# Kernel tuning notes

Hardware: AMD Instinct MI355X
Metric: run time of the kernel (lower is better)

## Reference

```python
import jax, jax.numpy as jnp
import numpy as np

B, D, CIN, H, W = 2, 6, 3, 96, 96
DIM, NUM_HEADS, DEPTH = 144, 6, 2
WS = (2, 8, 8)   # window size (d, h, w)
SS = (1, 4, 4)   # shift size for odd blocks
HID = int(DIM * 2.0)
TBL = (2 * WS[0] - 1) * (2 * WS[1] - 1) * (2 * WS[2] - 1)  # 675
EPS = 1e-5


def _rpi(ws):
    # pairwise relative position index, same math as WindowAttention.get_position_index
    coords = np.stack(np.meshgrid(np.arange(ws[0]), np.arange(ws[1]), np.arange(ws[2]), indexing='ij'))
    cf = coords.reshape(3, -1).astype(np.int64)
    rc = (cf[:, :, None] - cf[:, None, :]).transpose(1, 2, 0)
    rc[..., 0] += ws[0] - 1
    rc[..., 1] += ws[1] - 1
    rc[..., 2] += ws[2] - 1
    rc[..., 0] *= (2 * ws[1] - 1) * (2 * ws[2] - 1)
    rc[..., 1] *= 2 * ws[2] - 1
    return rc.sum(-1)  # (N, N)


def _win_part_np(x, ws):
    b, d, h, w, c = x.shape
    x = x.reshape(b, d // ws[0], ws[0], h // ws[1], ws[1], w // ws[2], ws[2], c)
    return x.transpose(0, 1, 3, 5, 2, 4, 6, 7).reshape(-1, ws[0] * ws[1] * ws[2], c)


def _attn_mask(Dp, Hp, Wp, ws, ss):
    # static shift-window attention mask, same as compute_mask
    img = np.zeros((1, Dp, Hp, Wp, 1), np.float32)
    cnt = 0
    for d in (slice(-ws[0]), slice(-ws[0], -ss[0]), slice(-ss[0], None)):
        for h in (slice(-ws[1]), slice(-ws[1], -ss[1]), slice(-ss[1], None)):
            for w in (slice(-ws[2]), slice(-ws[2], -ss[2]), slice(-ss[2], None)):
                img[:, d, h, w, :] = cnt
                cnt += 1
    mw = _win_part_np(img, ws)[..., 0]  # (nW, N)
    am = mw[:, None, :] - mw[:, :, None]
    return np.where(am != 0, np.float32(-100.0), np.float32(0.0))


RPI = jnp.asarray(_rpi(WS))            # (N, N) int
MASK = jnp.asarray(_attn_mask(D, H, W, WS, SS))  # (nW, N, N)


def _ln(x, g, b):
    mu = jnp.mean(x, -1, keepdims=True)
    var = jnp.mean(jnp.square(x - mu), -1, keepdims=True)
    return (x - mu) * jax.lax.rsqrt(var + EPS) * g + b


def _win_part(x, ws):
    b, d, h, w, c = x.shape
    x = x.reshape(b, d // ws[0], ws[0], h // ws[1], ws[1], w // ws[2], ws[2], c)
    return x.transpose(0, 1, 3, 5, 2, 4, 6, 7).reshape(-1, ws[0] * ws[1] * ws[2], c)


def _win_rev(xw, ws, b, d, h, w):
    x = xw.reshape(b, d // ws[0], h // ws[1], w // ws[2], ws[0], ws[1], ws[2], -1)
    return x.transpose(0, 1, 4, 2, 5, 3, 6, 7).reshape(b, d, h, w, -1)


def _stl(x, i, shifted, params):
    # one Swin Transformer Layer; x: (B, D, H, W, C)
    n1g, n1b, qkvw, qkvb, rpb, projw, projb, n2g, n2b, fc1w, fc1b, fc2w, fc2b = params
    b, d, h, w, c = x.shape
    hd = c // NUM_HEADS
    scale = hd ** -0.5
    y = _ln(x, n1g[i], n1b[i])
    if shifted:
        y = jnp.roll(y, (-SS[0], -SS[1], -SS[2]), axis=(1, 2, 3))
    xw = _win_part(y, WS)  # (B_, N, C)
    B_, N, _ = xw.shape
    qkv = jnp.einsum('bnc,oc->bno', xw, qkvw[i]) + qkvb[i]
    qkv = qkv.reshape(B_, N, 3, NUM_HEADS, hd).transpose(2, 0, 3, 1, 4)
    q, k, v = qkv[0], qkv[1], qkv[2]
    attn = jnp.einsum('bhnd,bhmd->bhnm', q * scale, k)
    bias = rpb[i][RPI].transpose(2, 0, 1)  # (heads, N, N)
    attn = attn + bias[None]
    if shifted:
        nW = MASK.shape[0]
        attn = attn.reshape(B_ // nW, nW, NUM_HEADS, N, N) + MASK[None, :, None]
        attn = attn.reshape(B_, NUM_HEADS, N, N)
    attn = jax.nn.softmax(attn, axis=-1)
    out = jnp.einsum('bhnm,bhmd->bhnd', attn, v).transpose(0, 2, 1, 3).reshape(B_, N, c)
    out = jnp.einsum('bnc,oc->bno', out, projw[i]) + projb[i]
    y = _win_rev(out, WS, b, d, h, w)
    if shifted:
        y = jnp.roll(y, (SS[0], SS[1], SS[2]), axis=(1, 2, 3))
    x = x + y
    z = _ln(x, n2g[i], n2b[i])
    z = jnp.einsum('bdhwc,oc->bdhwo', z, fc1w[i]) + fc1b[i]
    z = jax.nn.gelu(z, approximate=False)
    z = jnp.einsum('bdhwo,co->bdhwc', z, fc2w[i]) + fc2b[i]
    return x + z


def setup_inputs() -> dict:
    key = jax.random.key(0)
    ks = jax.random.split(key, 8)
    s = 0.02
    return {
        'x': jax.random.normal(ks[0], (B, D, CIN, H, W), jnp.float32),
        'conv_w': jax.random.normal(ks[1], (DIM, CIN, 1, 3, 3), jnp.float32) * s,
        'conv_b': jnp.zeros((DIM,), jnp.float32),
        'ln0_g': jnp.ones((DIM,), jnp.float32),
        'ln0_b': jnp.zeros((DIM,), jnp.float32),
        'n1g': jnp.ones((DEPTH, DIM), jnp.float32),
        'n1b': jnp.zeros((DEPTH, DIM), jnp.float32),
        'qkvw': jax.random.normal(ks[2], (DEPTH, 3 * DIM, DIM), jnp.float32) * s,
        'qkvb': jnp.zeros((DEPTH, 3 * DIM), jnp.float32),
        'rpb': jax.random.normal(ks[3], (DEPTH, TBL, NUM_HEADS), jnp.float32) * s,
        'projw': jax.random.normal(ks[4], (DEPTH, DIM, DIM), jnp.float32) * s,
        'projb': jnp.zeros((DEPTH, DIM), jnp.float32),
        'n2g': jnp.ones((DEPTH, DIM), jnp.float32),
        'n2b': jnp.zeros((DEPTH, DIM), jnp.float32),
        'fc1w': jax.random.normal(ks[5], (DEPTH, HID, DIM), jnp.float32) * s,
        'fc1b': jnp.zeros((DEPTH, HID), jnp.float32),
        'fc2w': jax.random.normal(ks[6], (DEPTH, DIM, HID), jnp.float32) * s,
        'fc2b': jnp.zeros((DEPTH, DIM), jnp.float32),
        'lin_w': jax.random.normal(ks[7], (DIM, DIM), jnp.float32) * s,
        'lin_b': jnp.zeros((DIM,), jnp.float32),
        'ln1_g': jnp.ones((DIM,), jnp.float32),
        'ln1_b': jnp.zeros((DIM,), jnp.float32),
    }


def reference(x, conv_w, conv_b, ln0_g, ln0_b, n1g, n1b, qkvw, qkvb, rpb, projw, projb,
              n2g, n2b, fc1w, fc1b, fc2w, fc2b, lin_w, lin_b, ln1_g, ln1_b):
    # x: (n, d, c, h, w)
    y = x.transpose(0, 2, 1, 3, 4)  # n c d h w
    y = jax.lax.conv_general_dilated(
        y, conv_w, (1, 1, 1), [(0, 0), (1, 1), (1, 1)],
        dimension_numbers=('NCDHW', 'OIDHW', 'NCDHW')) + conv_b[None, :, None, None, None]
    y = y.transpose(0, 2, 3, 4, 1)  # n d h w c
    y = _ln(y, ln0_g, ln0_b)
    y = y.transpose(0, 4, 1, 2, 3)  # n c d h w
    params = (n1g, n1b, qkvw, qkvb, rpb, projw, projb, n2g, n2b, fc1w, fc1b, fc2w, fc2b)
    # RSTB (num_blocks = 1): residual group (STG of DEPTH STLs) + linear + skip
    f = y.transpose(0, 2, 3, 4, 1)  # b d h w c
    for i in range(DEPTH):
        f = _stl(f, i, i % 2 == 1, params)
    f = jnp.einsum('bdhwc,oc->bdhwo', f, lin_w) + lin_b
    y = y + f.transpose(0, 4, 1, 2, 3)
    # trailing LayerNorm and rearrange back to (n, d, c, h, w)
    out = _ln(y.transpose(0, 2, 3, 4, 1), ln1_g, ln1_b)
    return out.transpose(0, 1, 4, 2, 3)
```

## Files before the change

kernel.cpp:

```cpp
#include <hip/hip_runtime.h>
#include <math.h>

#define NTOK 110592
#define NWIN 864
#define TS   15925248

typedef unsigned short u16;
typedef unsigned int   u32;
typedef __attribute__((ext_vector_type(8))) short short8;
typedef __attribute__((ext_vector_type(4))) float float4v;

__device__ __forceinline__ float bf2f(u16 v) { return __uint_as_float(((u32)v) << 16); }
__device__ __forceinline__ u16 f2bf(float f) {
    u32 u = __float_as_uint(f);
    u32 r = u + 0x7fffu + ((u >> 16) & 1u);
    return (u16)(r >> 16);
}
__device__ __forceinline__ void unpack2(u32 u, float& lo, float& hi) {
    lo = __uint_as_float(u << 16);
    hi = __uint_as_float(u & 0xffff0000u);
}
__device__ __forceinline__ u32 pack2(float lo, float hi) {
    return (u32)f2bf(lo) | ((u32)f2bf(hi) << 16);
}
__device__ __forceinline__ float wave_sum(float v) {
    #pragma unroll
    for (int o = 32; o > 0; o >>= 1) v += __shfl_xor(v, o, 64);
    return v;
}

__device__ __forceinline__ void win_to_src(int tw, int shifted, int& sb, int& sd, int& sh, int& sw) {
    int n = tw & 127;
    int win = tw >> 7;
    int ww = win % 12;
    int wh = (win / 12) % 12;
    int rest = win / 144;
    int wd = rest % 3;
    sb = rest / 3;
    int ld = n >> 6, lh = (n >> 3) & 7, lw = n & 7;
    int dr = wd * 2 + ld, hr = wh * 8 + lh, wr = ww * 8 + lw;
    if (shifted) {
        sd = (dr + 1) % 6;
        sh = (hr + 4) % 96;
        sw = (wr + 4) % 96;
    } else {
        sd = dr; sh = hr; sw = wr;
    }
}

__device__ __forceinline__ int tok_region(int t, int wdn, int whn, int wwn) {
    int dr = wdn * 2 + (t >> 6), hr = whn * 8 + ((t >> 3) & 7), wr = wwn * 8 + (t & 7);
    int rd = (dr < 4) ? 0 : ((dr < 5) ? 1 : 2);
    int rh = (hr < 88) ? 0 : ((hr < 92) ? 1 : 2);
    int rw = (wr < 88) ? 0 : ((wr < 92) ? 1 : 2);
    return rd * 9 + rh * 3 + rw;
}

__global__ __launch_bounds__(256) void convert_weights(
    const float* __restrict__ qkvw, const float* __restrict__ projw,
    const float* __restrict__ fc1w, const float* __restrict__ fc2w,
    const float* __restrict__ linw, u16* __restrict__ wbuf,
    const float* __restrict__ rpb, float* __restrict__ bexp)
{
    int i = blockIdx.x * 256 + threadIdx.x;
    if (i < 124416) wbuf[i] = f2bf(qkvw[i]);
    else if (i < 165888) wbuf[i] = f2bf(projw[i - 124416]);
    else if (i < 248832) wbuf[i] = f2bf(fc1w[i - 165888]);
    else if (i < 331776) wbuf[i] = f2bf(fc2w[i - 248832]);
    else if (i < 352512) wbuf[i] = f2bf(linw[i - 331776]);
    else if (i < 549120) {
        int k = i - 352512;
        int n = k & 127, m = (k >> 7) & 127;
        int lh = k >> 14;
        int h = lh % 6, l = lh / 6;
        int rdi = (m >> 6) - (n >> 6) + 1;
        int rhi = ((m >> 3) & 7) - ((n >> 3) & 7) + 7;
        int rwi = (m & 7) - (n & 7) + 7;
        int bi = (rdi * 15 + rhi) * 15 + rwi;
        bexp[k] = rpb[l * 4050 + bi * 6 + h];
    }
}

__global__ __launch_bounds__(256) void conv_ln0_row(
    const float* __restrict__ x, const float* __restrict__ cw, const float* __restrict__ cb,
    const float* __restrict__ g0, const float* __restrict__ b0,
    float* __restrict__ y0)
{
    int bh = blockIdx.x;
    int h = bh % 96, bd = bh / 96;
    int b = bd / 6, d = bd - b * 6;
    __shared__ float ws[192][29];
    __shared__ float xsr[9][100];
    __shared__ float cbias[192], gg[144], bbv[144];
    int tid = threadIdx.x;

    for (int i = tid; i < 9 * 98; i += 256) {
        int row = i / 98, wx = i - row * 98;
        int ci = row / 3, kh = row - 3 * ci;
        int hh = h + kh - 1, wsrc = wx - 1;
        float v = 0.f;
        if (hh >= 0 && hh < 96 && wsrc >= 0 && wsrc < 96)
            v = x[((((size_t)b * 6 + d) * 3 + ci) * 96 + hh) * 96 + wsrc];
        xsr[row][wx] = v;
    }
    for (int i = tid; i < 192 * 27; i += 256) {
        int c = i / 27, j = i - c * 27;
        ws[c][j] = (c < 144) ? cw[c * 27 + j] : 0.f;
    }
    for (int i = tid; i < 192; i += 256) cbias[i] = (i < 144) ? cb[i] : 0.f;
    for (int i = tid; i < 144; i += 256) { gg[i] = g0[i]; bbv[i] = b0[i]; }
    __syncthreads();

    int wv = tid >> 6, lane = tid & 63;
    int p0 = wv * 24;

    float a0[24], a1[24], a2[24];
    #pragma unroll
    for (int k = 0; k < 24; k++) {
        a0[k] = cbias[lane]; a1[k] = cbias[lane + 64]; a2[k] = cbias[lane + 128];
    }

    for (int cikh = 0; cikh < 9; cikh++) {
        const float* xr = &xsr[cikh][p0];
        float xv[26];
        #pragma unroll
        for (int t = 0; t < 26; t++) xv[t] = xr[t];
        #pragma unroll
        for (int kw = 0; kw < 3; kw++) {
            int j = cikh * 3 + kw;
            float w0 = ws[lane][j], w1 = ws[lane + 64][j], w2 = ws[lane + 128][j];
            #pragma unroll
            for (int k = 0; k < 24; k++) {
                float xvv = xv[k + kw];
                a0[k] += w0 * xvv; a1[k] += w1 * xvv; a2[k] += w2 * xvv;
            }
        }
    }

    #pragma unroll
    for (int k = 0; k < 24; k++) {
        int p = p0 + k;
        float v0 = a0[k], v1 = a1[k];
        float v2m = (lane < 16) ? a2[k] : 0.f;
        float s  = wave_sum(v0 + v1 + v2m);
        float s2 = wave_sum(v0 * v0 + v1 * v1 + v2m * v2m);
        float mu = s * (1.f / 144.f);
        float rstd = rsqrtf(fmaxf(s2 * (1.f / 144.f) - mu * mu, 0.f) + 1e-5f);
        size_t o = ((size_t)bh * 96 + p) * 144;
        float r0 = (v0 - mu) * rstd * gg[lane] + bbv[lane];
        float r1 = (v1 - mu) * rstd * gg[lane + 64] + bbv[lane + 64];
        y0[o + lane] = r0;
        y0[o + lane + 64] = r1;
        if (lane < 16) {
            float r2 = (a2[k] - mu) * rstd * gg[lane + 128] + bbv[lane + 128];
            y0[o + lane + 128] = r2;
        }
    }
}

template<int MODE>
__global__ __launch_bounds__(256) void ln_gather(
    const float* __restrict__ in, u16* __restrict__ out,
    const float* __restrict__ g, const float* __restrict__ bt)
{
    int tok = blockIdx.x * 4 + (threadIdx.x >> 6);
    int lane = threadIdx.x & 63;
    int src;
    if (MODE == 0) src = tok;
    else {
        int b, d, h, w;
        win_to_src(tok, MODE == 2, b, d, h, w);
        src = ((b * 6 + d) * 96 + h) * 96 + w;
    }
    const float2* row = (const float2*)(in + (size_t)src * 144);
    float2 a = row[lane];
    float2 b2 = (lane < 8) ? row[64 + lane] : make_float2(0.f, 0.f);
    float s  = wave_sum(a.x + a.y + b2.x + b2.y);
    float s2 = wave_sum(a.x * a.x + a.y * a.y + b2.x * b2.x + b2.y * b2.y);
    float mu = s * (1.f / 144.f);
    float rstd = rsqrtf(fmaxf(s2 * (1.f / 144.f) - mu * mu, 0.f) + 1e-5f);
    const float2* g2 = (const float2*)g;
    const float2* t2 = (const float2*)bt;
    u32* orow = (u32*)(out + (size_t)tok * 144);
    float2 gg = g2[lane], tt = t2[lane];
    orow[lane] = pack2((a.x - mu) * rstd * gg.x + tt.x, (a.y - mu) * rstd * gg.y + tt.y);
    if (lane < 8) {
        float2 gh = g2[64 + lane], th = t2[64 + lane];
        orow[64 + lane] = pack2((b2.x - mu) * rstd * gh.x + th.x, (b2.y - mu) * rstd * gh.y + th.y);
    }
}

template<int AMODE, int EPI, int SHIFTED, int ADDBIAS, int KTILES>
__global__ __launch_bounds__(192) void mgemm(
    const void* __restrict__ Asrc, const u16* __restrict__ Wt, const float* __restrict__ bias,
    u16* __restrict__ outb, float* __restrict__ fres, const float* __restrict__ y0,
    int a_add, int a_ld, int w_ld, int o_ld, int o_add)
{
    __shared__ u16 As[64 * 152];
    int m0 = blockIdx.y * 64, n0 = blockIdx.x * 144;
    int tid = threadIdx.x;
    int wv3 = tid / 64, lane = tid & 63;
    int mrow = lane & 15, quad = lane >> 4;
    const short8 z8 = {0, 0, 0, 0, 0, 0, 0, 0};

    float4v acc[4][3];
    #pragma unroll
    for (int i = 0; i < 4; i++)
        #pragma unroll
        for (int j = 0; j < 3; j++) acc[i][j] = (float4v){0.f, 0.f, 0.f, 0.f};

    #pragma unroll
    for (int kt = 0; kt < KTILES; kt++) {
        if (kt) __syncthreads();
        if (AMODE == 2) {
            const u16* A = (const u16*)Asrc;
            #pragma unroll
            for (int idx = tid; idx < 1152; idx += 192) {
                int r = idx / 18, c4 = idx - r * 18;
                *(short8*)&As[r * 152 + c4 * 8] =
                    *(const short8*)&A[(size_t)(a_add + m0 + r) * a_ld + kt * 144 + c4 * 8];
            }
        } else if (AMODE == 3) {
            const u16* A = (const u16*)Asrc;
            int chtok = a_ld;
            int cc = m0 / chtok;
            int t0 = m0 - cc * chtok;
            const u16* Ac = A + (size_t)cc * chtok * 144;
            #pragma unroll
            for (int idx = tid; idx < 1152; idx += 192) {
                int r = idx / 18, c4 = idx - r * 18;
                int hh = c4 / 3, sub = c4 - hh * 3;
                *(short8*)&As[r * 152 + c4 * 8] =
                    *(const short8*)&Ac[((size_t)hh * chtok + t0 + r) * 24 + sub * 8];
            }
        } else {
            const float* A = (const float*)Asrc;
            #pragma unroll
            for (int idx = tid; idx < 2304; idx += 192) {
                int r = idx / 36, c4 = idx - r * 36;
                const float4* src4 = (const float4*)&A[(size_t)(a_add + m0 + r) * a_ld + kt * 144];
                float4 v = src4[c4];
                *(u32*)&As[r * 152 + c4 * 4]     = pack2(v.x, v.y);
                *(u32*)&As[r * 152 + c4 * 4 + 2] = pack2(v.z, v.w);
            }
        }
        __syncthreads();

        const u16* Wg = Wt + (size_t)(n0 + wv3 * 48 + mrow) * w_ld + kt * 144;

        #pragma unroll
        for (int ks = 0; ks < 4; ks++) {
            int k0 = ks * 32;
            short8 af[4], bf[3];
            #pragma unroll
            for (int i = 0; i < 4; i++)
                af[i] = *(const short8*)&As[(i * 16 + mrow) * 152 + k0 + quad * 8];
            #pragma unroll
            for (int j = 0; j < 3; j++)
                bf[j] = *(const short8*)&Wg[(size_t)j * 16 * w_ld + k0 + quad * 8];
            #pragma unroll
            for (int i = 0; i < 4; i++)
                #pragma unroll
                for (int j = 0; j < 3; j++)
                    acc[i][j] = __builtin_amdgcn_mfma_f32_16x16x32_bf16(af[i], bf[j], acc[i][j], 0, 0, 0);
        }
        {
            bool tl = (quad < 2);
            short8 af[4], bf[3];
            #pragma unroll
            for (int i = 0; i < 4; i++)
                af[i] = tl ? *(const short8*)&As[(i * 16 + mrow) * 152 + 128 + quad * 8] : z8;
            #pragma unroll
            for (int j = 0; j < 3; j++)
                bf[j] = tl ? *(const short8*)&Wg[(size_t)j * 16 * w_ld + 128 + quad * 8] : z8;
            #pragma unroll
            for (int i = 0; i < 4; i++)
                #pragma unroll
                for (int j = 0; j < 3; j++)
                    acc[i][j] = __builtin_amdgcn_mfma_f32_16x16x32_bf16(af[i], bf[j], acc[i][j], 0, 0, 0);
        }
    }

    #pragma unroll
    for (int i = 0; i < 4; i++) {
        #pragma unroll
        for (int reg = 0; reg < 4; reg++) {
            int m = m0 + i * 16 + quad * 4 + reg;
            int orow;
            if (EPI == 2 || EPI == 5) {
                int b, d, h, w;
                win_to_src(m, SHIFTED, b, d, h, w);
                orow = ((b * 6 + d) * 96 + h) * 96 + w;
            } else orow = m + o_add;
            #pragma unroll
            for (int j = 0; j < 3; j++) {
                int n = n0 + wv3 * 48 + j * 16 + mrow;
                float v = acc[i][j][reg];
                if (ADDBIAS) v += bias[n];
                if (EPI == 1) v = 0.5f * v * (1.f + erff(v * 0.70710678118f));
                if (EPI == 2 || EPI == 3) {
                    fres[(size_t)orow * 144 + n] += v;
                } else if (EPI == 5) {
                    fres[(size_t)orow * 144 + n] = y0[(size_t)orow * 144 + n] + v;
                } else if (EPI == 6) {
                    int slot = n / 144;
                    int hn = n - slot * 144;
                    int head = hn / 24, dd = hn - head * 24;
                    if (slot == 0) v *= 0.20412414523193154f;
                    outb[((size_t)head * o_ld + orow) * 72 + slot * 24 + dd] = f2bf(v);
                } else {
                    if (EPI == 4) v += y0[(size_t)orow * o_ld + n];
                    outb[(size_t)orow * o_ld + n] = f2bf(v);
                }
            }
        }
    }
}

template<int SHIFTED>
__global__ __launch_bounds__(256) void attn_mfma(
    const u16* __restrict__ qkv,
    const float* __restrict__ bexp,
    u16* __restrict__ tok_out,
    int win_base, int chtok)
{
    int win = blockIdx.x;
    int head = blockIdx.y;
    __shared__ __align__(16) u16 Pb[4][2048];
    __shared__ __align__(16) u16 Vt[3072];
    __shared__ float invden_s[128];
    __shared__ u32 reg_pack[32];

    int tid = threadIdx.x;
    int wv = tid >> 6, lane = tid & 63;
    int c = lane & 15, quad = lane >> 4;
    int qbase = wv * 32;
    const short8 z8 = {0, 0, 0, 0, 0, 0, 0, 0};
    const float* bh_ = bexp + head * 16384;
    const u16* base = qkv + ((size_t)head * chtok + (size_t)win * 128) * 72;
    int cs = (c & 7) << 3;

    int wdn = 0, whn = 0, wwn = 0;
    if (SHIFTED) {
        int wib = (win_base + win) % 432;
        wwn = wib % 12; whn = (wib / 12) % 12; wdn = wib / 144;
    }

    if (tid < 128) {
        const u32* vsrc = (const u32*)(base + (size_t)tid * 72 + 48);
        #pragma unroll
        for (int i = 0; i < 12; i++) {
            u32 u = vsrc[i];
            int d0 = 2 * i, d1 = 2 * i + 1;
            Vt[((d0 << 7) + tid) ^ ((d0 & 7) << 3)] = (u16)(u & 0xffffu);
            Vt[((d1 << 7) + tid) ^ ((d1 & 7) << 3)] = (u16)(u >> 16);
        }
    }
    if (SHIFTED && tid < 32) {
        int t0 = tid * 4;
        reg_pack[tid] = (u32)tok_region(t0, wdn, whn, wwn)
                      | ((u32)tok_region(t0 + 1, wdn, whn, wwn) << 8)
                      | ((u32)tok_region(t0 + 2, wdn, whn, wwn) << 16)
                      | ((u32)tok_region(t0 + 3, wdn, whn, wwn) << 24);
    }
    __syncthreads();

    short8 aq[2];
    #pragma unroll
    for (int i = 0; i < 2; i++) {
        aq[i] = z8;
        if (quad < 3)
            aq[i] = *(const short8*)(base + (size_t)(qbase + i * 16 + c) * 72 + quad * 8);
    }

    float4v s_acc[2][8];
    #pragma unroll
    for (int i = 0; i < 2; i++)
        #pragma unroll
        for (int j = 0; j < 8; j++) s_acc[i][j] = (float4v){0.f, 0.f, 0.f, 0.f};

    #pragma unroll
    for (int j = 0; j < 8; j++) {
        short8 kf = z8;
        if (quad < 3)
            kf = *(const short8*)(base + (size_t)(j * 16 + c) * 72 + 24 + quad * 8);
        s_acc[0][j] = __builtin_amdgcn_mfma_f32_16x16x32_bf16(kf, aq[0], s_acc[0][j], 0, 0, 0);
        s_acc[1][j] = __builtin_amdgcn_mfma_f32_16x16x32_bf16(kf, aq[1], s_acc[1][j], 0, 0, 0);
    }

    float4v o_acc[2][2];
    #pragma unroll
    for (int i = 0; i < 2; i++)
        #pragma unroll
        for (int jv = 0; jv < 2; jv++) o_acc[i][jv] = (float4v){0.f, 0.f, 0.f, 0.f};

    #pragma unroll
    for (int i = 0; i < 2; i++) {
        int m = qbase + i * 16 + c;
        const float* brow = bh_ + m * 128;
        u32 myreg = SHIFTED ? (u32)tok_region(m, wdn, whn, wwn) : 0u;
        float den = 0.f;
        #pragma unroll
        for (int j = 0; j < 8; j++) {
            float4 bv = *(const float4*)(brow + j * 16 + quad * 4);
            float s0 = s_acc[i][j][0] + bv.x;
            float s1 = s_acc[i][j][1] + bv.y;
            float s2 = s_acc[i][j][2] + bv.z;
            float s3 = s_acc[i][j][3] + bv.w;
            if (SHIFTED) {
                u32 rv = reg_pack[j * 4 + quad];
                s0 += ((rv & 255u) == myreg) ? 0.f : -100.f;
                s1 += (((rv >> 8) & 255u) == myreg) ? 0.f : -100.f;
                s2 += (((rv >> 16) & 255u) == myreg) ? 0.f : -100.f;
                s3 += ((rv >> 24) == myreg) ? 0.f : -100.f;
            }
            float p0 = __expf(s0), p1 = __expf(s1), p2 = __expf(s2), p3 = __expf(s3);
            den += (p0 + p1) + (p2 + p3);
            u32 w0, w1;
            asm("v_cvt_pk_bf16_f32 %0, %1, %2" : "=v"(w0) : "v"(p0), "v"(p1));
            asm("v_cvt_pk_bf16_f32 %0, %1, %2" : "=v"(w1) : "v"(p2), "v"(p3));
            uint2 wpair = make_uint2(w0, w1);
            *(uint2*)&Pb[wv][((c << 7) + j * 16 + quad * 4) ^ cs] = wpair;
        }
        den += __shfl_xor(den, 16, 64);
        den += __shfl_xor(den, 32, 64);
        if (quad == 0) invden_s[m] = 1.f / den;

        #pragma unroll
        for (int ks = 0; ks < 4; ks++) {
            short8 pf  = *(const short8*)&Pb[wv][((c << 7) + ks * 32 + quad * 8) ^ cs];
            short8 vf0 = *(const short8*)&Vt[((c << 7) + ks * 32 + quad * 8) ^ cs];
            short8 vf1 = (c < 8) ? *(const short8*)&Vt[(((16 + c) << 7) + ks * 32 + quad * 8) ^ cs] : z8;
            o_acc[i][0] = __builtin_amdgcn_mfma_f32_16x16x32_bf16(pf, vf0, o_acc[i][0], 0, 0, 0);
            o_acc[i][1] = __builtin_amdgcn_mfma_f32_16x16x32_bf16(pf, vf1, o_acc[i][1], 0, 0, 0);
        }
    }

    float* ob = (float*)&Pb[wv][0];
    #pragma unroll
    for (int i = 0; i < 2; i++)
        #pragma unroll
        for (int jv = 0; jv < 2; jv++) {
            int d = jv * 16 + c;
            if (d < 24) {
                #pragma unroll
                for (int r = 0; r < 4; r++)
                    ob[(i * 16 + quad * 4 + r) * 26 + d] = o_acc[i][jv][r];
            }
        }
    __syncthreads();

    if (tid < 128) {
        const float2* ol = (const float2*)((const float*)&Pb[0][0]
                                           + (tid >> 5) * 1024 + (tid & 31) * 26);
        float inv = invden_s[tid];
        u32* orow = (u32*)tok_out + ((size_t)head * chtok + (size_t)win * 128 + tid) * 12;
        #pragma unroll
        for (int d2 = 0; d2 < 12; d2++) {
            float2 v = ol[d2];
            orow[d2] = pack2(v.x * inv, v.y * inv);
        }
    }
}

__global__ __launch_bounds__(256) void final_ln_out_kernel(
    const u16* __restrict__ gsrc, const float* __restrict__ g, const float* __restrict__ bt,
    float* __restrict__ out)
{
    int bh = blockIdx.x;
    int h = bh % 96, d = (bh / 96) % 6, b = bh / 576;
    __shared__ u16 tile[96][152];
    __shared__ float stat[96][2];
    const u16* src = gsrc + (size_t)bh * 96 * 144;
    for (int i = threadIdx.x; i < 1728; i += 256) {
        int wt = i / 18, c8 = i - wt * 18;
        *(short8*)&tile[wt][c8 * 8] = *(const short8*)&src[wt * 144 + c8 * 8];
    }
    __syncthreads();
    if (threadIdx.x < 96) {
        const u32* row = (const u32*)&tile[threadIdx.x][0];
        float s = 0.f, s2 = 0.f;
        #pragma unroll
        for (int j = 0; j < 72; j++) {
            float lo, hi; unpack2(row[j], lo, hi);
            s += lo + hi; s2 += lo * lo + hi * hi;
        }
        float mu = s * (1.f / 144.f);
        float var = s2 * (1.f / 144.f) - mu * mu;
        stat[threadIdx.x][0] = mu;
        stat[threadIdx.x][1] = rsqrtf(fmaxf(var, 0.f) + 1e-5f);
    }
    __syncthreads();
    size_t obase = ((size_t)(b * 6 + d) * 144) * 9216 + h * 96;
    for (int i = threadIdx.x; i < 96 * 144; i += blockDim.x) {
        int c = i / 96, wt = i - c * 96;
        out[obase + (size_t)c * 9216 + wt] =
            (bf2f(tile[wt][c]) - stat[wt][0]) * stat[wt][1] * g[c] + bt[c];
    }
}

extern "C" void kernel_launch(void* const* d_in, const int* in_sizes, int n_in,
                              void* d_out, int out_size, void* d_ws, size_t ws_size,
                              hipStream_t stream) {
    const float* x     = (const float*)d_in[0];
    const float* convw = (const float*)d_in[1];
    const float* convb = (const float*)d_in[2];
    const float* ln0g  = (const float*)d_in[3];
    const float* ln0b  = (const float*)d_in[4];
    const float* n1g   = (const float*)d_in[5];
    const float* n1b   = (const float*)d_in[6];
    const float* qkvw  = (const float*)d_in[7];
    const float* qkvb  = (const float*)d_in[8];
    const float* rpb   = (const float*)d_in[9];
    const float* projw = (const float*)d_in[10];
    const float* projb = (const float*)d_in[11];
    const float* n2g   = (const float*)d_in[12];
    const float* n2b   = (const float*)d_in[13];
    const float* fc1w  = (const float*)d_in[14];
    const float* fc1b  = (const float*)d_in[15];
    const float* fc2w  = (const float*)d_in[16];
    const float* fc2b  = (const float*)d_in[17];
    const float* linw  = (const float*)d_in[18];
    const float* linb  = (const float*)d_in[19];
    const float* ln1g  = (const float*)d_in[20];
    const float* ln1b  = (const float*)d_in[21];

    char* wp = (char*)d_ws;
    float* f    = (float*)wp;             wp += (size_t)TS * 4;
    u16*   tok  = (u16*)wp;               wp += (size_t)TS * 2;
    u16*   wbuf = (u16*)wp;               wp += 352512ull * 2;
    float* bexp = (float*)wp;             wp += 196608ull * 4;
    u16*   qkvbuf = (u16*)wp;
    size_t rest = ws_size - (size_t)(wp - (char*)d_ws);
    int nch = (rest >= (size_t)NTOK * 432 * 2) ? 1
            : (rest >= (size_t)NTOK * 216 * 2) ? 2 : 4;
    int nm  = (rest >= (size_t)NTOK * 288 * 2) ? 1
            : (rest >= (size_t)NTOK * 144 * 2) ? 2 : 3;
    float* y0 = (float*)d_out;

    convert_weights<<<2145, 256, 0, stream>>>(qkvw, projw, fc1w, fc2w, linw, wbuf, rpb, bexp);
    conv_ln0_row<<<1152, 256, 0, stream>>>(x, convw, convb, ln0g, ln0b, y0);

    for (int layer = 0; layer < 2; ++layer) {
        const u16* qw  = wbuf + (size_t)layer * 62208;
        const u16* pw  = wbuf + 124416 + (size_t)layer * 20736;
        const u16* f1w = wbuf + 165888 + (size_t)layer * 41472;
        const u16* f2w = wbuf + 248832 + (size_t)layer * 41472;
        const float* qb  = qkvb + (size_t)layer * 432;
        const float* pb  = projb + (size_t)layer * 144;
        const float* g1  = n1g + layer * 144;
        const float* b1  = n1b + layer * 144;
        const float* g2  = n2g + layer * 144;
        const float* b2  = n2b + layer * 144;
        const float* f1b = fc1b + (size_t)layer * 288;
        const float* f2b = fc2b + (size_t)layer * 144;
        const float* bx  = bexp + (size_t)layer * 98304;

        if (layer == 0) ln_gather<1><<<NTOK / 4, 256, 0, stream>>>(y0, tok, g1, b1);
        else            ln_gather<2><<<NTOK / 4, 256, 0, stream>>>(f, tok, g1, b1);

        int chtok = NTOK / nch, chwin = NWIN / nch;
        for (int c = 0; c < nch; c++) {
            mgemm<2, 6, 0, 1, 1><<<dim3(3, chtok / 64), 192, 0, stream>>>(
                tok, qw, qb, qkvbuf, nullptr, nullptr,
                c * chtok, 144, 144, chtok, 0);
            u16* ob = tok + (size_t)c * chtok * 144;
            if (layer == 0)
                attn_mfma<0><<<dim3(chwin, 6), 256, 0, stream>>>(qkvbuf, bx, ob, c * chwin, chtok);
            else
                attn_mfma<1><<<dim3(chwin, 6), 256, 0, stream>>>(qkvbuf, bx, ob, c * chwin, chtok);
        }

        if (layer == 0)
            mgemm<3, 5, 0, 1, 1><<<dim3(1, NTOK / 64), 192, 0, stream>>>(
                tok, pw, pb, nullptr, f, y0, 0, chtok, 144, 144, 0);
        else
            mgemm<3, 2, 1, 1, 1><<<dim3(1, NTOK / 64), 192, 0, stream>>>(
                tok, pw, pb, nullptr, f, nullptr, 0, chtok, 144, 144, 0);

        ln_gather<0><<<NTOK / 4, 256, 0, stream>>>(f, tok, g2, b2);

        int fcch = NTOK / nm;
        for (int c = 0; c < nm; c++) {
            int mst = c * fcch;
            mgemm<2, 1, 0, 1, 1><<<dim3(2, fcch / 64), 192, 0, stream>>>(
                tok, f1w, f1b, qkvbuf, nullptr, nullptr, mst, 144, 144, 288, 0);
            mgemm<2, 3, 0, 1, 2><<<dim3(1, fcch / 64), 192, 0, stream>>>(
                qkvbuf, f2w, f2b, nullptr, f, nullptr, 0, 288, 288, 144, mst);
        }
    }

    mgemm<0, 4, 0, 1, 1><<<dim3(1, NTOK / 64), 192, 0, stream>>>(
        f, wbuf + 331776, linb, tok, nullptr, y0, 0, 144, 144, 144, 0);

    final_ln_out_kernel<<<2 * 6 * 96, 256, 0, stream>>>(tok, ln1g, ln1b, (float*)d_out);
}
```

Before: 839.9 us.

## Fuse LayerNorm into FC1 GEMM and stage QKV output through LDS

Removes the separate ln_gather<0> pass before the MLP: the FC1 GEMM now reads fp32 residual rows directly, computes the LayerNorm in its A-tile load and writes bf16 into shared memory. The QKV GEMM epilogue stages results in LDS and writes them coalesced into a new slot-major layout (Q, K, V planes per head), and attention reads Q/K/V from the separate planes. This trades an extra memory pass for recomputing the LayerNorm in both FC1 column blocks and adds extra syncs in the QKV epilogue. ln_gather's MODE 0 path now also goes through window remapping, but that mode is no longer launched.

```diff
diff --git a/kernel.cpp b/kernel.cpp
--- a/kernel.cpp
+++ b/kernel.cpp
@@ -166,8 +166,7 @@
     int tok = blockIdx.x * 4 + (threadIdx.x >> 6);
     int lane = threadIdx.x & 63;
     int src;
-    if (MODE == 0) src = tok;
-    else {
+    {
         int b, d, h, w;
         win_to_src(tok, MODE == 2, b, d, h, w);
         src = ((b * 6 + d) * 96 + h) * 96 + w;
@@ -194,6 +193,7 @@
 __global__ __launch_bounds__(192) void mgemm(
     const void* __restrict__ Asrc, const u16* __restrict__ Wt, const float* __restrict__ bias,
     u16* __restrict__ outb, float* __restrict__ fres, const float* __restrict__ y0,
+    const float* __restrict__ lng, const float* __restrict__ lnb,
     int a_add, int a_ld, int w_ld, int o_ld, int o_add)
 {
     __shared__ u16 As[64 * 152];
@@ -212,7 +212,36 @@
     #pragma unroll
     for (int kt = 0; kt < KTILES; kt++) {
         if (kt) __syncthreads();
-        if (AMODE == 2) {
+        if constexpr (AMODE == 5) {
+            __shared__ float gs[144], bs[144], ps[64][6];
+            for (int i = tid; i < 144; i += 192) { gs[i] = lng[i]; bs[i] = lnb[i]; }
+            int r = tid / 3, p = tid - 3 * r;
+            int srow = a_add + m0 + r;
+            const float4* s4 = (const float4*)((const float*)Asrc + (size_t)srow * 144) + p * 12;
+            float4 av[12];
+            float s = 0.f, s2 = 0.f;
+            #pragma unroll
+            for (int q = 0; q < 12; q++) {
+                av[q] = s4[q];
+                s  += (av[q].x + av[q].y) + (av[q].z + av[q].w);
+                s2 += (av[q].x * av[q].x + av[q].y * av[q].y)
+                    + (av[q].z * av[q].z + av[q].w * av[q].w);
+            }
+            ps[r][p] = s; ps[r][3 + p] = s2;
+            __syncthreads();
+            float S  = ps[r][0] + ps[r][1] + ps[r][2];
+            float S2 = ps[r][3] + ps[r][4] + ps[r][5];
+            float mu = S * (1.f / 144.f);
+            float rstd = rsqrtf(fmaxf(S2 * (1.f / 144.f) - mu * mu, 0.f) + 1e-5f);
+            #pragma unroll
+            for (int q = 0; q < 12; q++) {
+                int n = p * 48 + q * 4;
+                *(u32*)&As[r * 152 + n]     = pack2((av[q].x - mu) * rstd * gs[n]     + bs[n],
+                                                    (av[q].y - mu) * rstd * gs[n + 1] + bs[n + 1]);
+                *(u32*)&As[r * 152 + n + 2] = pack2((av[q].z - mu) * rstd * gs[n + 2] + bs[n + 2],
+                                                    (av[q].w - mu) * rstd * gs[n + 3] + bs[n + 3]);
+            }
+        } else if constexpr (AMODE == 2) {
             const u16* A = (const u16*)Asrc;
             #pragma unroll
             for (int idx = tid; idx < 1152; idx += 192) {
@@ -220,7 +249,7 @@
                 *(short8*)&As[r * 152 + c4 * 8] =
                     *(const short8*)&A[(size_t)(a_add + m0 + r) * a_ld + kt * 144 + c4 * 8];
             }
-        } else if (AMODE == 3) {
+        } else if constexpr (AMODE == 3) {
             const u16* A = (const u16*)Asrc;
             int chtok = a_ld;
             int cc = m0 / chtok;
@@ -281,36 +310,59 @@
         }
     }
 
-    #pragma unroll
-    for (int i = 0; i < 4; i++) {
-        #pragma unroll
-        for (int reg = 0; reg < 4; reg++) {
-            int m = m0 + i * 16 + quad * 4 + reg;
-            int orow;
-            if (EPI == 2 || EPI == 5) {
-                int b, d, h, w;
-                win_to_src(m, SHIFTED, b, d, h, w);
-                orow = ((b * 6 + d) * 96 + h) * 96 + w;
-            } else orow = m + o_add;
-            #pragma unroll
-            for (int j = 0; j < 3; j++) {
-                int n = n0 + wv3 * 48 + j * 16 + mrow;
-                float v = acc[i][j][reg];
-                if (ADDBIAS) v += bias[n];
-                if (EPI == 1) v = 0.5f * v * (1.f + erff(v * 0.70710678118f));
-                if (EPI == 2 || EPI == 3) {
-                    fres[(size_t)orow * 144 + n] += v;
-                } else if (EPI == 5) {
-                    fres[(size_t)orow * 144 + n] = y0[(size_t)orow * 144 + n] + v;
-                } else if (EPI == 6) {
-                    int slot = n / 144;
-                    int hn = n - slot * 144;
-                    int head = hn / 24, dd = hn - head * 24;
+    if constexpr (EPI == 6) {
+        __syncthreads();
+        int slot = blockIdx.x;
+        #pragma unroll
+        for (int i = 0; i < 4; i++)
+            #pragma unroll
+            for (int reg = 0; reg < 4; reg++) {
+                int ml = i * 16 + quad * 4 + reg;
+                #pragma unroll
+                for (int j = 0; j < 3; j++) {
+                    int hn = wv3 * 48 + j * 16 + mrow;
+                    float v = acc[i][j][reg];
+                    if (ADDBIAS) v += bias[n0 + hn];
                     if (slot == 0) v *= 0.20412414523193154f;
-                    outb[((size_t)head * o_ld + orow) * 72 + slot * 24 + dd] = f2bf(v);
-                } else {
-                    if (EPI == 4) v += y0[(size_t)orow * o_ld + n];
-                    outb[(size_t)orow * o_ld + n] = f2bf(v);
+                    As[ml * 152 + hn] = f2bf(v);
+                }
+            }
+        __syncthreads();
+        int chtok = o_ld;
+        u32* outw = (u32*)outb;
+        for (int gi = tid; gi < 4608; gi += 192) {
+            int hh = gi / 768;
+            int rem = gi - hh * 768;
+            int t = rem / 12, dd2 = rem - t * 12;
+            outw[(size_t)slot * 72 * chtok + ((size_t)hh * chtok + m0 + t) * 12 + dd2]
+                = *(const u32*)&As[t * 152 + hh * 24 + dd2 * 2];
+        }
+    } else {
+        #pragma unroll
+        for (int i = 0; i < 4; i++) {
+            #pragma unroll
+            for (int reg = 0; reg < 4; reg++) {
+                int m = m0 + i * 16 + quad * 4 + reg;
+                int orow;
+                if (EPI == 2 || EPI == 5) {
+                    int b, d, h, w;
+                    win_to_src(m, SHIFTED, b, d, h, w);
+                    orow = ((b * 6 + d) * 96 + h) * 96 + w;
+                } else orow = m + o_add;
+                #pragma unroll
+                for (int j = 0; j < 3; j++) {
+                    int n = n0 + wv3 * 48 + j * 16 + mrow;
+                    float v = acc[i][j][reg];
+                    if (ADDBIAS) v += bias[n];
+                    if (EPI == 1) v = 0.5f * v * (1.f + erff(v * 0.70710678118f));
+                    if (EPI == 2 || EPI == 3) {
+                        fres[(size_t)orow * 144 + n] += v;
+                    } else if (EPI == 5) {
+                        fres[(size_t)orow * 144 + n] = y0[(size_t)orow * 144 + n] + v;
+                    } else {
+                        if (EPI == 4) v += y0[(size_t)orow * o_ld + n];
+                        outb[(size_t)orow * o_ld + n] = f2bf(v);
+                    }
                 }
             }
         }
@@ -337,7 +389,9 @@
     int qbase = wv * 32;
     const short8 z8 = {0, 0, 0, 0, 0, 0, 0, 0};
     const float* bh_ = bexp + head * 16384;
-    const u16* base = qkv + ((size_t)head * chtok + (size_t)win * 128) * 72;
+    const u16* qb_ = qkv + ((size_t)head * chtok + (size_t)win * 128) * 24;
+    const u16* kb_ = qb_ + (size_t)144 * chtok;
+    const u16* vb_ = qb_ + (size_t)288 * chtok;
     int cs = (c & 7) << 3;
 
     int wdn = 0, whn = 0, wwn = 0;
@@ -347,7 +401,7 @@
     }
 
     if (tid < 128) {
-        const u32* vsrc = (const u32*)(base + (size_t)tid * 72 + 48);
+        const u32* vsrc = (const u32*)(vb_ + (size_t)tid * 24);
         #pragma unroll
         for (int i = 0; i < 12; i++) {
             u32 u = vsrc[i];
@@ -370,7 +424,7 @@
     for (int i = 0; i < 2; i++) {
         aq[i] = z8;
         if (quad < 3)
-            aq[i] = *(const short8*)(base + (size_t)(qbase + i * 16 + c) * 72 + quad * 8);
+            aq[i] = *(const short8*)(qb_ + (size_t)(qbase + i * 16 + c) * 24 + quad * 8);
     }
 
     float4v s_acc[2][8];
@@ -383,7 +437,7 @@
     for (int j = 0; j < 8; j++) {
         short8 kf = z8;
         if (quad < 3)
-            kf = *(const short8*)(base + (size_t)(j * 16 + c) * 72 + 24 + quad * 8);
+            kf = *(const short8*)(kb_ + (size_t)(j * 16 + c) * 24 + quad * 8);
         s_acc[0][j] = __builtin_amdgcn_mfma_f32_16x16x32_bf16(kf, aq[0], s_acc[0][j], 0, 0, 0);
         s_acc[1][j] = __builtin_amdgcn_mfma_f32_16x16x32_bf16(kf, aq[1], s_acc[1][j], 0, 0, 0);
     }
@@ -562,7 +616,7 @@
         int chtok = NTOK / nch, chwin = NWIN / nch;
         for (int c = 0; c < nch; c++) {
             mgemm<2, 6, 0, 1, 1><<<dim3(3, chtok / 64), 192, 0, stream>>>(
-                tok, qw, qb, qkvbuf, nullptr, nullptr,
+                tok, qw, qb, qkvbuf, nullptr, nullptr, nullptr, nullptr,
                 c * chtok, 144, 144, chtok, 0);
             u16* ob = tok + (size_t)c * chtok * 144;
             if (layer == 0)
@@ -573,25 +627,23 @@
 
         if (layer == 0)
             mgemm<3, 5, 0, 1, 1><<<dim3(1, NTOK / 64), 192, 0, stream>>>(
-                tok, pw, pb, nullptr, f, y0, 0, chtok, 144, 144, 0);
+                tok, pw, pb, nullptr, f, y0, nullptr, nullptr, 0, chtok, 144, 144, 0);
         else
             mgemm<3, 2, 1, 1, 1><<<dim3(1, NTOK / 64), 192, 0, stream>>>(
-                tok, pw, pb, nullptr, f, nullptr, 0, chtok, 144, 144, 0);
-
-        ln_gather<0><<<NTOK / 4, 256, 0, stream>>>(f, tok, g2, b2);
+                tok, pw, pb, nullptr, f, nullptr, nullptr, nullptr, 0, chtok, 144, 144, 0);
 
         int fcch = NTOK / nm;
         for (int c = 0; c < nm; c++) {
             int mst = c * fcch;
-            mgemm<2, 1, 0, 1, 1><<<dim3(2, fcch / 64), 192, 0, stream>>>(
-                tok, f1w, f1b, qkvbuf, nullptr, nullptr, mst, 144, 144, 288, 0);
+            mgemm<5, 1, 0, 1, 1><<<dim3(2, fcch / 64), 192, 0, stream>>>(
+                f, f1w, f1b, qkvbuf, nullptr, nullptr, g2, b2, mst, 144, 144, 288, 0);
             mgemm<2, 3, 0, 1, 2><<<dim3(1, fcch / 64), 192, 0, stream>>>(
-                qkvbuf, f2w, f2b, nullptr, f, nullptr, 0, 288, 288, 144, mst);
+                qkvbuf, f2w, f2b, nullptr, f, nullptr, nullptr, nullptr, 0, 288, 288, 144, mst);
         }
     }
 
     mgemm<0, 4, 0, 1, 1><<<dim3(1, NTOK / 64), 192, 0, stream>>>(
-        f, wbuf + 331776, linb, tok, nullptr, y0, 0, 144, 144, 144, 0);
+        f, wbuf + 331776, linb, tok, nullptr, y0, nullptr, nullptr, 0, 144, 144, 144, 0);
 
     final_ln_out_kernel<<<2 * 6 * 96, 256, 0, stream>>>(tok, ln1g, ln1b, (float*)d_out);
 }
```

Result: faster. 789.6 us (-6.0%).
